# Performance work log

Measured on AMD Instinct MI355X. Metric: run time of the kernel, lower is better.

Reference implementation:

```python
import jax, jax.numpy as jnp
import numpy as np

TOPK_CONF = 100   # cfg.nms_top_k_conf
TOPK_IOU = 15     # cfg.nms_top_k_iou
IOU_GAUSS = (32, 32)  # cfg.iou_gauss_dim
EPS = 1e-6        # cfg.positive


def unnormal_gaussian(mask_shape, loc):
    """loc: [..., 4] = (cx, cy, w, h) in [0,1). Returns [..., H, W] unnormalized gaussians."""
    H, W = mask_shape
    ys = (jnp.arange(H, dtype=loc.dtype) + 0.5) / H  # [H]
    xs = (jnp.arange(W, dtype=loc.dtype) + 0.5) / W  # [W]
    cx, cy = loc[..., 0], loc[..., 1]
    sx = jnp.abs(loc[..., 2]) * 0.5 + 1e-3
    sy = jnp.abs(loc[..., 3]) * 0.5 + 1e-3
    dx2 = (xs - cx[..., None]) ** 2 / (2.0 * sx[..., None] ** 2)  # [..., W]
    dy2 = (ys - cy[..., None]) ** 2 / (2.0 * sy[..., None] ** 2)  # [..., H]
    return jnp.exp(-(dy2[..., :, None] + dx2[..., None, :]))      # [..., H, W]


def setup_inputs() -> dict:
    key = jax.random.key(0)
    k1, k2, k3, k4, k5 = jax.random.split(key, 5)
    B, P, C, M = 4, 19248, 81, 32
    original = jax.random.normal(k1, (B, 3, 550, 550), dtype=jnp.float32)
    loc = jax.random.uniform(k2, (B, P, 4), dtype=jnp.float32)  # cx,cy,w,h in [0,1)
    conf = jax.random.normal(k3, (B, P, C), dtype=jnp.float32)
    mask = jax.random.normal(k4, (B, P, M), dtype=jnp.float32)
    proto = jax.random.normal(k5, (B, 138, 138, M), dtype=jnp.float32)
    return {"original": original, "loc": loc, "conf": conf, "mask": mask, "proto": proto}


def reference(original, loc, conf, mask, proto):
    B, H, W = original.shape[0], original.shape[2], original.shape[3]
    # class-1 foreground confidence after softmax over classes
    conf1 = jax.nn.softmax(conf, axis=2)[:, :, 1]  # [B, P]

    # ---- detect(): top-k by conf, pairwise gaussian IoU, keep lowest-overlap boxes ----
    order = jnp.argsort(-conf1, axis=-1)[:, :TOPK_CONF]                    # [B, K]
    sconf = jnp.take_along_axis(conf1, order, axis=1)                      # [B, K]
    sloc = jnp.take_along_axis(loc, order[..., None], axis=1)              # [B, K, 4]
    smask = jnp.take_along_axis(mask, order[..., None], axis=1)            # [B, K, Mdim]

    gauss = unnormal_gaussian(IOU_GAUSS, sloc)                             # [B, K, G, G]
    g_rows = gauss[:, None, :, :, :]                                       # broadcast [B,1,K,G,G]
    g_cols = gauss[:, :, None, :, :]                                       # broadcast [B,K,1,G,G]
    inter = jnp.sum(jnp.minimum(g_rows, g_cols), axis=(-2, -1))            # [B, K, K]
    union = jnp.sum(jnp.maximum(g_rows, g_cols), axis=(-2, -1))            # [B, K, K]
    gauss_iou = inter / union
    iou_max = jnp.max(jnp.triu(gauss_iou, k=1), axis=1)                    # [B, K]
    keep = jnp.argsort(iou_max, axis=-1)[:, :TOPK_IOU]                     # [B, Kk]

    kloc = jnp.take_along_axis(sloc, keep[..., None], axis=1)              # [B, Kk, 4]
    kmask = jnp.take_along_axis(smask, keep[..., None], axis=1)            # [B, Kk, Mdim]
    kconf = jnp.take_along_axis(sconf, keep, axis=1)                       # [B, Kk]

    # ---- VarianceLoss ----
    Hp, Wp = proto.shape[1], proto.shape[2]
    ug = unnormal_gaussian((Hp, Wp), kloc)                                 # [B, Kk, Hp, Wp]
    assembled = jax.nn.sigmoid(jnp.einsum('bhwm,bkm->bkhw', proto, kmask)) # lincomb + sigmoid
    attention = assembled * ug
    mask_conf = attention * kconf[:, :, None, None]                        # einsum('abcd,ab->abcd')
    denom = jnp.sum(mask_conf, axis=1, keepdims=True) + EPS
    final_conf = 1.0 - jnp.sum(mask_conf ** 2 / denom, axis=1)             # [B, Hp, Wp]
    final_conf = jnp.where(jnp.isnan(final_conf), 0.0, final_conf)

    resized = jax.image.resize(final_conf, (B, H, W), method='bilinear')   # [B, H, W]
    total_conf = jnp.sum(resized, axis=0)                                  # [H, W]
    weighted_mean = jnp.einsum('bchw,bhw->chw', original, resized)         # [C, H, W]
    squared_diff = (original - weighted_mean) ** 2
    weighted_diff = squared_diff * resized[:, None, :, :]                  # einsum('abcd,acd->abcd')
    weighted_var = weighted_diff / (total_conf + EPS)
    return jnp.sum(weighted_var) / 100.0
```

## Files before the change

### kernel.cpp

```cpp
#include <hip/hip_runtime.h>
#include <math.h>

#define B 4
#define P 19248
#define C 81
#define M 32
#define K1 100
#define K2 15
#define G 32
#define HP 138
#define HO 550
#define FEPS 1e-6f
#define NLOC 19

#define NBUCKET 8192
#define CAP 2048

#define TI 16
#define NT 7
#define NTP 28
#define CH 128
#define NCH 8
#define SP 132

__global__ void k_conf1(const float* __restrict__ conf, float* __restrict__ conf1) {
    int gid  = blockIdx.x * blockDim.x + threadIdx.x;
    int wave = gid >> 6;
    int lane = threadIdx.x & 63;
    if (wave >= B * P) return;
    const float* row = conf + (size_t)wave * C;
    float x0 = (lane < C)      ? row[lane]      : -INFINITY;
    float x1 = (lane + 64 < C) ? row[lane + 64] : -INFINITY;
    float m = fmaxf(x0, x1);
#pragma unroll
    for (int o = 32; o; o >>= 1) m = fmaxf(m, __shfl_xor(m, o, 64));
    float s = 0.f;
    if (lane < C)      s += expf(x0 - m);
    if (lane + 64 < C) s += expf(x1 - m);
#pragma unroll
    for (int o = 32; o; o >>= 1) s += __shfl_xor(s, o, 64);
    if (lane == 0) conf1[wave] = expf(row[1] - m) / s;
}

__global__ __launch_bounds__(1024) void k_top100(
    const float* __restrict__ conf1, const float* __restrict__ loc,
    const float* __restrict__ mask,
    float* __restrict__ sconf, float* __restrict__ sloc,
    float* __restrict__ smask) {
    int b = blockIdx.x;
    int tid = threadIdx.x;
    const float* c1 = conf1 + (size_t)b * P;

    __shared__ unsigned int hist[NBUCKET];
    __shared__ unsigned int gsum_[1024];
    __shared__ unsigned int g2[64];
    __shared__ unsigned long long keys[CAP];
    __shared__ int s_T;
    __shared__ int s_cnt;
    __shared__ int   s_order[K1];
    __shared__ float s_conf[K1];

    for (int i = tid; i < NBUCKET; i += 1024) hist[i] = 0;
    if (tid == 0) s_cnt = 0;
    __syncthreads();

    unsigned int mybits[NLOC];
#pragma unroll
    for (int s = 0; s < NLOC; ++s) {
        int p = tid + s * 1024;
        mybits[s] = (p < P) ? __float_as_uint(c1[p]) : 0u;
        if (p < P) atomicAdd(&hist[mybits[s] >> 17], 1u);
    }
    __syncthreads();

    {
        unsigned int gs = 0;
#pragma unroll
        for (int i = 0; i < 8; ++i) gs += hist[tid * 8 + i];
        gsum_[tid] = gs;
    }
    __syncthreads();
    if (tid < 64) {
        unsigned int gs = 0;
#pragma unroll
        for (int i = 0; i < 16; ++i) gs += gsum_[tid * 16 + i];
        g2[tid] = gs;
    }
    __syncthreads();

    if (tid == 0) {
        int cum = 0;
        int S = 63;
        for (; S > 0; --S) {
            if (cum + (int)g2[S] >= K1) break;
            cum += (int)g2[S];
        }
        int gI = S * 16 + 15;
        for (; gI > S * 16; --gI) {
            if (cum + (int)gsum_[gI] >= K1) break;
            cum += (int)gsum_[gI];
        }
        int T = gI * 8 + 7;
        for (; T > gI * 8; --T) {
            cum += (int)hist[T];
            if (cum >= K1) break;
        }
        s_T = T;
    }
    __syncthreads();

    int T = s_T;
#pragma unroll
    for (int s = 0; s < NLOC; ++s) {
        int p = tid + s * 1024;
        if (p < P && (int)(mybits[s] >> 17) >= T) {
            int pos = atomicAdd(&s_cnt, 1);
            if (pos < CAP)
                keys[pos] = ((unsigned long long)mybits[s] << 32)
                          | (unsigned int)(0xFFFFFFFFu - (unsigned int)p);
        }
    }
    __syncthreads();
    int nc = min(s_cnt, CAP);

    if (tid < nc) {
        unsigned long long mk = keys[tid];
        int rank = 0;
        for (int i = 0; i < nc; ++i) rank += (keys[i] > mk);
        if (rank < K1) {
            unsigned int bits = (unsigned int)(mk >> 32);
            int idx = (int)(0xFFFFFFFFu - (unsigned int)(mk & 0xFFFFFFFFu));
            s_order[rank] = idx;
            s_conf[rank] = __uint_as_float(bits);
        }
    }
    __syncthreads();

    for (int t = tid; t < K1; t += 1024) {
        sconf[b * K1 + t] = s_conf[t];
    }
    for (int t = tid; t < K1 * 4; t += 1024) {
        int k = t >> 2, d = t & 3;
        sloc[(b * K1 + k) * 4 + d] = loc[((size_t)b * P + s_order[k]) * 4 + d];
    }
    for (int t = tid; t < K1 * M; t += 1024) {
        int k = t >> 5, d = t & 31;
        smask[(b * K1 + k) * M + d] = mask[((size_t)b * P + s_order[k]) * M + d];
    }
}

__global__ void k_gauss(const float* __restrict__ sloc, float* __restrict__ gauss,
                        unsigned int* __restrict__ ioumax, float* __restrict__ out) {
    int bk = blockIdx.x;
    if (threadIdx.x == 0) ioumax[bk] = 0u;
    if (bk == 0 && threadIdx.x == 1) out[0] = 0.f;
    const float* l = sloc + bk * 4;
    float cx = l[0], cy = l[1];
    float sx = fabsf(l[2]) * 0.5f + 0.001f;
    float sy = fabsf(l[3]) * 0.5f + 0.001f;
    float dsx = 2.f * sx * sx;
    float dsy = 2.f * sy * sy;
    for (int p = threadIdx.x; p < G * G; p += 256) {
        int y = p >> 5, x = p & 31;
        float xs = (x + 0.5f) / (float)G;
        float ys = (y + 0.5f) / (float)G;
        float dx2 = (xs - cx) * (xs - cx) / dsx;
        float dy2 = (ys - cy) * (ys - cy) / dsy;
        gauss[(size_t)bk * (G * G) + p] = expf(-(dy2 + dx2));
    }
}

__global__ __launch_bounds__(256) void k_iou(
    const float* __restrict__ gauss, unsigned int* __restrict__ ioumax) {
    int tp = blockIdx.x;
    int b  = blockIdx.y;
    int ti = 0, rem = tp;
    while (rem >= NT - ti) { rem -= NT - ti; ++ti; }
    int tj = ti + rem;

    __shared__ __align__(16) float As[TI][SP];
    __shared__ __align__(16) float Bs[TI][SP];

    int tid = threadIdx.x;
    int li = tid >> 4, lj = tid & 15;
    int i = ti * TI + li, j = tj * TI + lj;

    float inter = 0.f, uni = 0.f;
    for (int ch = 0; ch < NCH; ++ch) {
        __syncthreads();
        for (int idx = tid; idx < TI * (CH / 4); idx += 256) {
            int g = idx >> 5, v = idx & 31;
            int gi = ti * TI + g;
            float4 f = make_float4(0.f, 0.f, 0.f, 0.f);
            if (gi < K1)
                f = *(const float4*)(gauss + ((size_t)(b * K1 + gi) << 10) + ch * CH + v * 4);
            *(float4*)(&As[g][v * 4]) = f;
            int gj = tj * TI + g;
            float4 h = make_float4(0.f, 0.f, 0.f, 0.f);
            if (gj < K1)
                h = *(const float4*)(gauss + ((size_t)(b * K1 + gj) << 10) + ch * CH + v * 4);
            *(float4*)(&Bs[g][v * 4]) = h;
        }
        __syncthreads();
        const float4* ar = (const float4*)(&As[li][0]);
        const float4* br = (const float4*)(&Bs[lj][0]);
#pragma unroll
        for (int p = 0; p < CH / 4; ++p) {
            float4 a = ar[p], c = br[p];
            inter += fminf(a.x, c.x) + fminf(a.y, c.y)
                   + fminf(a.z, c.z) + fminf(a.w, c.w);
            uni   += fmaxf(a.x, c.x) + fmaxf(a.y, c.y)
                   + fmaxf(a.z, c.z) + fmaxf(a.w, c.w);
        }
    }
    if (i < j && j < K1) {
        float iou = inter / uni;
        atomicMax(&ioumax[b * K1 + j], __float_as_uint(iou));
    }
}

__global__ void k_keep(const unsigned int* __restrict__ ioumax,
                       const float* __restrict__ sloc, const float* __restrict__ smask,
                       const float* __restrict__ sconf,
                       float* __restrict__ kloc, float* __restrict__ kmask,
                       float* __restrict__ kconf) {
    int b = blockIdx.x;
    int lane = threadIdx.x;
    float v0 = (lane < K1)      ? __uint_as_float(ioumax[b * K1 + lane])      : INFINITY;
    float v1 = (lane + 64 < K1) ? __uint_as_float(ioumax[b * K1 + lane + 64]) : INFINITY;
    __shared__ int s_keep[K2];
    for (int k = 0; k < K2; ++k) {
        float bv; int bi;
        if (v0 <= v1) { bv = v0; bi = lane; }
        else          { bv = v1; bi = lane + 64; }
#pragma unroll
        for (int o = 32; o; o >>= 1) {
            float ov = __shfl_xor(bv, o, 64);
            int   oi = __shfl_xor(bi, o, 64);
            if (ov < bv || (ov == bv && oi < bi)) { bv = ov; bi = oi; }
        }
        if (bi == lane)           v0 = INFINITY;
        else if (bi == lane + 64) v1 = INFINITY;
        if (lane == 0) s_keep[k] = bi;
    }
    __syncthreads();
    for (int t = lane; t < K2 * M; t += 64) {
        int k = t >> 5, d = t & 31;
        kmask[(b * K2 + k) * M + d] = smask[(b * K1 + s_keep[k]) * M + d];
    }
    for (int t = lane; t < K2 * 4; t += 64) {
        int k = t >> 2, d = t & 3;
        kloc[(b * K2 + k) * 4 + d] = sloc[(b * K1 + s_keep[k]) * 4 + d];
    }
    if (lane < K2) kconf[b * K2 + lane] = sconf[b * K1 + s_keep[lane]];
}

__global__ __launch_bounds__(256) void k_fconf(
    const float* __restrict__ proto, const float* __restrict__ kloc,
    const float* __restrict__ kmask, const float* __restrict__ kconf,
    float* __restrict__ fconf) {
    int b = blockIdx.y;
    int px0 = blockIdx.x * 256;
    int tid = threadIdx.x;
    __shared__ float s_pv[256][M + 1];
    __shared__ float s_km[K2][M];
    __shared__ float s_loc[K2][4];
    __shared__ float s_cf[K2];
    for (int t = tid; t < K2 * M; t += 256) s_km[t >> 5][t & 31] = kmask[b * K2 * M + t];
    for (int t = tid; t < K2 * 4; t += 256) s_loc[t >> 2][t & 3] = kloc[b * K2 * 4 + t];
    if (tid < K2) s_cf[tid] = kconf[b * K2 + tid];

    int nvalid = min(256, HP * HP - px0);
    const float4* pr4 = (const float4*)(proto + ((size_t)b * (HP * HP) + px0) * M);
    for (int idx = tid; idx < nvalid * (M / 4); idx += 256) {
        float4 f = pr4[idx];
        int q = idx >> 3, v = idx & 7;
        s_pv[q][v * 4 + 0] = f.x;
        s_pv[q][v * 4 + 1] = f.y;
        s_pv[q][v * 4 + 2] = f.z;
        s_pv[q][v * 4 + 3] = f.w;
    }
    __syncthreads();

    if (tid < nvalid) {
        int p = px0 + tid;
        int h = p / HP, w = p % HP;
        float pv[M];
#pragma unroll
        for (int m = 0; m < M; ++m) pv[m] = s_pv[tid][m];
        float ys = (h + 0.5f) / (float)HP;
        float xs = (w + 0.5f) / (float)HP;
        float sum_a = 0.f, sum_a2 = 0.f;
#pragma unroll 1
        for (int k = 0; k < K2; ++k) {
            float d = 0.f;
#pragma unroll
            for (int m = 0; m < M; ++m) d += pv[m] * s_km[k][m];
            float sig = 1.f / (1.f + expf(-d));
            float cx = s_loc[k][0], cy = s_loc[k][1];
            float sx = fabsf(s_loc[k][2]) * 0.5f + 0.001f;
            float sy = fabsf(s_loc[k][3]) * 0.5f + 0.001f;
            float dx2 = (xs - cx) * (xs - cx) / (2.f * sx * sx);
            float dy2 = (ys - cy) * (ys - cy) / (2.f * sy * sy);
            float ug = expf(-(dy2 + dx2));
            float a = sig * ug * s_cf[k];
            sum_a  += a;
            sum_a2 += a * a;
        }
        float fin = 1.f - sum_a2 / (sum_a + FEPS);
        if (!(fin == fin)) fin = 0.f;
        fconf[(size_t)b * HP * HP + p] = fin;
    }
}

__global__ void k_reduce(const float* __restrict__ fconf, const float* __restrict__ original,
                         float* __restrict__ out) {
    int idx = blockIdx.x * 256 + threadIdx.x;
    float contrib = 0.f;
    if (idx < HO * HO) {
        int y = idx / HO, x = idx % HO;
        const float scale = (float)HP / (float)HO;
        float fy = (y + 0.5f) * scale - 0.5f;
        float fx = (x + 0.5f) * scale - 0.5f;
        float y0f = floorf(fy), x0f = floorf(fx);
        float wy = fy - y0f, wx = fx - x0f;
        int y0 = (int)y0f, x0 = (int)x0f;
        int iy0 = max(y0, 0), iy1 = min(y0 + 1, HP - 1);
        int ix0 = max(x0, 0), ix1 = min(x0 + 1, HP - 1);
        float r[B];
#pragma unroll
        for (int b = 0; b < B; ++b) {
            const float* F = fconf + (size_t)b * HP * HP;
            float v00 = F[iy0 * HP + ix0], v01 = F[iy0 * HP + ix1];
            float v10 = F[iy1 * HP + ix0], v11 = F[iy1 * HP + ix1];
            r[b] = (1.f - wy) * ((1.f - wx) * v00 + wx * v01)
                 +        wy  * ((1.f - wx) * v10 + wx * v11);
        }
        float t = r[0] + r[1] + r[2] + r[3];
        float s = 0.f;
#pragma unroll
        for (int c = 0; c < 3; ++c) {
            float o[B], wm = 0.f;
#pragma unroll
            for (int b = 0; b < B; ++b) {
                o[b] = original[(((size_t)b * 3 + c) * HO + y) * HO + x];
                wm += o[b] * r[b];
            }
#pragma unroll
            for (int b = 0; b < B; ++b) {
                float d = o[b] - wm;
                s += d * d * r[b];
            }
        }
        contrib = s / (t + FEPS);
    }
    __shared__ float red[256];
    red[threadIdx.x] = contrib;
    __syncthreads();
    for (int off = 128; off; off >>= 1) {
        if (threadIdx.x < off) red[threadIdx.x] += red[threadIdx.x + off];
        __syncthreads();
    }
    if (threadIdx.x == 0) atomicAdd(out, red[0] * 0.01f);
}

extern "C" void kernel_launch(void* const* d_in, const int* in_sizes, int n_in,
                              void* d_out, int out_size, void* d_ws, size_t ws_size,
                              hipStream_t stream) {
    (void)in_sizes; (void)n_in; (void)out_size; (void)ws_size;
    const float* original = (const float*)d_in[0];
    const float* loc      = (const float*)d_in[1];
    const float* conf     = (const float*)d_in[2];
    const float* mask     = (const float*)d_in[3];
    const float* proto    = (const float*)d_in[4];
    float* out = (float*)d_out;

    char* ws = (char*)d_ws;
    size_t off = 0;
    auto alloc = [&](size_t bytes) -> void* {
        void* p = ws + off;
        off += (bytes + 255) & ~(size_t)255;
        return p;
    };
    float* conf1        = (float*)alloc((size_t)B * P * sizeof(float));
    float* sconf        = (float*)alloc((size_t)B * K1 * sizeof(float));
    float* sloc         = (float*)alloc((size_t)B * K1 * 4 * sizeof(float));
    float* smask        = (float*)alloc((size_t)B * K1 * M * sizeof(float));
    float* gauss        = (float*)alloc((size_t)B * K1 * G * G * sizeof(float));
    unsigned int* iomax = (unsigned int*)alloc((size_t)B * K1 * sizeof(unsigned int));
    float* kloc         = (float*)alloc((size_t)B * K2 * 4 * sizeof(float));
    float* kmask        = (float*)alloc((size_t)B * K2 * M * sizeof(float));
    float* kconf        = (float*)alloc((size_t)B * K2 * sizeof(float));
    float* fconf        = (float*)alloc((size_t)B * HP * HP * sizeof(float));

    k_conf1<<<(B * P) / 4, 256, 0, stream>>>(conf, conf1);
    k_top100<<<B, 1024, 0, stream>>>(conf1, loc, mask, sconf, sloc, smask);
    k_gauss<<<B * K1, 256, 0, stream>>>(sloc, gauss, iomax, out);
    dim3 g4(NTP, B);
    k_iou<<<g4, 256, 0, stream>>>(gauss, iomax);
    k_keep<<<B, 64, 0, stream>>>(iomax, sloc, smask, sconf, kloc, kmask, kconf);
    dim3 g6((HP * HP + 255) / 256, B);
    k_fconf<<<g6, 256, 0, stream>>>(proto, kloc, kmask, kconf, fconf);
    k_reduce<<<(HO * HO + 255) / 256, 256, 0, stream>>>(fconf, original, out);
}
```

Measured before the change: 188.0 us.

## Fuse gaussian generation into IoU kernel and keep-selection into fconf kernel

Drops the standalone gaussian kernel: each IoU tile now computes its gaussian values on the fly in shared memory from the box parameters, so the gauss buffer no longer goes through global memory. The top-15 keep selection moves into the start of every fconf block, and ioumax/out zeroing moves into the conf1 kernel. This removes two kernel launches and the intermediate buffers. In exchange the exp work is repeated across tiles and every fconf block repeats the selection.

```diff
diff --git a/kernel.cpp b/kernel.cpp
--- a/kernel.cpp
+++ b/kernel.cpp
@@ -23,7 +23,12 @@
 #define NCH 8
 #define SP 132
 
-__global__ void k_conf1(const float* __restrict__ conf, float* __restrict__ conf1) {
+__global__ void k_conf1(const float* __restrict__ conf, float* __restrict__ conf1,
+                        unsigned int* __restrict__ ioumax, float* __restrict__ out) {
+    if (blockIdx.x == 0) {
+        for (int t = threadIdx.x; t < B * K1; t += 256) ioumax[t] = 0u;
+        if (threadIdx.x == 0) out[0] = 0.f;
+    }
     int gid  = blockIdx.x * blockDim.x + threadIdx.x;
     int wave = gid >> 6;
     int lane = threadIdx.x & 63;
@@ -149,29 +154,8 @@
     }
 }
 
-__global__ void k_gauss(const float* __restrict__ sloc, float* __restrict__ gauss,
-                        unsigned int* __restrict__ ioumax, float* __restrict__ out) {
-    int bk = blockIdx.x;
-    if (threadIdx.x == 0) ioumax[bk] = 0u;
-    if (bk == 0 && threadIdx.x == 1) out[0] = 0.f;
-    const float* l = sloc + bk * 4;
-    float cx = l[0], cy = l[1];
-    float sx = fabsf(l[2]) * 0.5f + 0.001f;
-    float sy = fabsf(l[3]) * 0.5f + 0.001f;
-    float dsx = 2.f * sx * sx;
-    float dsy = 2.f * sy * sy;
-    for (int p = threadIdx.x; p < G * G; p += 256) {
-        int y = p >> 5, x = p & 31;
-        float xs = (x + 0.5f) / (float)G;
-        float ys = (y + 0.5f) / (float)G;
-        float dx2 = (xs - cx) * (xs - cx) / dsx;
-        float dy2 = (ys - cy) * (ys - cy) / dsy;
-        gauss[(size_t)bk * (G * G) + p] = expf(-(dy2 + dx2));
-    }
-}
-
 __global__ __launch_bounds__(256) void k_iou(
-    const float* __restrict__ gauss, unsigned int* __restrict__ ioumax) {
+    const float* __restrict__ sloc, unsigned int* __restrict__ ioumax) {
     int tp = blockIdx.x;
     int b  = blockIdx.y;
     int ti = 0, rem = tp;
@@ -180,26 +164,51 @@
 
     __shared__ __align__(16) float As[TI][SP];
     __shared__ __align__(16) float Bs[TI][SP];
+    __shared__ float pa[2][TI][4];
 
     int tid = threadIdx.x;
+    if (tid < 2 * TI) {
+        int which = tid >> 4, g = tid & 15;
+        int gi = (which ? tj : ti) * TI + g;
+        float cx = 0.f, cy = 0.f, dsx = 1.f, dsy = 1.f;
+        if (gi < K1) {
+            const float* l = sloc + (size_t)(b * K1 + gi) * 4;
+            cx = l[0]; cy = l[1];
+            float sx = fabsf(l[2]) * 0.5f + 0.001f;
+            float sy = fabsf(l[3]) * 0.5f + 0.001f;
+            dsx = 2.f * sx * sx;
+            dsy = 2.f * sy * sy;
+        }
+        pa[which][g][0] = cx; pa[which][g][1] = cy;
+        pa[which][g][2] = dsx; pa[which][g][3] = dsy;
+    }
+
     int li = tid >> 4, lj = tid & 15;
     int i = ti * TI + li, j = tj * TI + lj;
 
     float inter = 0.f, uni = 0.f;
     for (int ch = 0; ch < NCH; ++ch) {
         __syncthreads();
-        for (int idx = tid; idx < TI * (CH / 4); idx += 256) {
-            int g = idx >> 5, v = idx & 31;
-            int gi = ti * TI + g;
-            float4 f = make_float4(0.f, 0.f, 0.f, 0.f);
-            if (gi < K1)
-                f = *(const float4*)(gauss + ((size_t)(b * K1 + gi) << 10) + ch * CH + v * 4);
-            *(float4*)(&As[g][v * 4]) = f;
-            int gj = tj * TI + g;
-            float4 h = make_float4(0.f, 0.f, 0.f, 0.f);
-            if (gj < K1)
-                h = *(const float4*)(gauss + ((size_t)(b * K1 + gj) << 10) + ch * CH + v * 4);
-            *(float4*)(&Bs[g][v * 4]) = h;
+#pragma unroll
+        for (int t = 0; t < TI * CH / 256; ++t) {
+            int idx = tid + t * 256;
+            int g = idx >> 7, px = idx & 127;
+            int p = ch * CH + px;
+            int y = p >> 5, x = p & 31;
+            float xs = (x + 0.5f) / (float)G;
+            float ys = (y + 0.5f) / (float)G;
+            {
+                float cx = pa[0][g][0], cy = pa[0][g][1];
+                float dx2 = (xs - cx) * (xs - cx) / pa[0][g][2];
+                float dy2 = (ys - cy) * (ys - cy) / pa[0][g][3];
+                As[g][px] = expf(-(dy2 + dx2));
+            }
+            {
+                float cx = pa[1][g][0], cy = pa[1][g][1];
+                float dx2 = (xs - cx) * (xs - cx) / pa[1][g][2];
+                float dy2 = (ys - cy) * (ys - cy) / pa[1][g][3];
+                Bs[g][px] = expf(-(dy2 + dx2));
+            }
         }
         __syncthreads();
         const float4* ar = (const float4*)(&As[li][0]);
@@ -219,46 +228,10 @@
     }
 }
 
-__global__ void k_keep(const unsigned int* __restrict__ ioumax,
-                       const float* __restrict__ sloc, const float* __restrict__ smask,
-                       const float* __restrict__ sconf,
-                       float* __restrict__ kloc, float* __restrict__ kmask,
-                       float* __restrict__ kconf) {
-    int b = blockIdx.x;
-    int lane = threadIdx.x;
-    float v0 = (lane < K1)      ? __uint_as_float(ioumax[b * K1 + lane])      : INFINITY;
-    float v1 = (lane + 64 < K1) ? __uint_as_float(ioumax[b * K1 + lane + 64]) : INFINITY;
-    __shared__ int s_keep[K2];
-    for (int k = 0; k < K2; ++k) {
-        float bv; int bi;
-        if (v0 <= v1) { bv = v0; bi = lane; }
-        else          { bv = v1; bi = lane + 64; }
-#pragma unroll
-        for (int o = 32; o; o >>= 1) {
-            float ov = __shfl_xor(bv, o, 64);
-            int   oi = __shfl_xor(bi, o, 64);
-            if (ov < bv || (ov == bv && oi < bi)) { bv = ov; bi = oi; }
-        }
-        if (bi == lane)           v0 = INFINITY;
-        else if (bi == lane + 64) v1 = INFINITY;
-        if (lane == 0) s_keep[k] = bi;
-    }
-    __syncthreads();
-    for (int t = lane; t < K2 * M; t += 64) {
-        int k = t >> 5, d = t & 31;
-        kmask[(b * K2 + k) * M + d] = smask[(b * K1 + s_keep[k]) * M + d];
-    }
-    for (int t = lane; t < K2 * 4; t += 64) {
-        int k = t >> 2, d = t & 3;
-        kloc[(b * K2 + k) * 4 + d] = sloc[(b * K1 + s_keep[k]) * 4 + d];
-    }
-    if (lane < K2) kconf[b * K2 + lane] = sconf[b * K1 + s_keep[lane]];
-}
-
 __global__ __launch_bounds__(256) void k_fconf(
-    const float* __restrict__ proto, const float* __restrict__ kloc,
-    const float* __restrict__ kmask, const float* __restrict__ kconf,
-    float* __restrict__ fconf) {
+    const float* __restrict__ proto, const unsigned int* __restrict__ ioumax,
+    const float* __restrict__ sloc, const float* __restrict__ smask,
+    const float* __restrict__ sconf, float* __restrict__ fconf) {
     int b = blockIdx.y;
     int px0 = blockIdx.x * 256;
     int tid = threadIdx.x;
@@ -266,9 +239,38 @@
     __shared__ float s_km[K2][M];
     __shared__ float s_loc[K2][4];
     __shared__ float s_cf[K2];
-    for (int t = tid; t < K2 * M; t += 256) s_km[t >> 5][t & 31] = kmask[b * K2 * M + t];
-    for (int t = tid; t < K2 * 4; t += 256) s_loc[t >> 2][t & 3] = kloc[b * K2 * 4 + t];
-    if (tid < K2) s_cf[tid] = kconf[b * K2 + tid];
+    __shared__ int s_keep[K2];
+
+    if (tid < 64) {
+        int lane = tid;
+        float v0 = (lane < K1)      ? __uint_as_float(ioumax[b * K1 + lane])      : INFINITY;
+        float v1 = (lane + 64 < K1) ? __uint_as_float(ioumax[b * K1 + lane + 64]) : INFINITY;
+        for (int k = 0; k < K2; ++k) {
+            float bv; int bi;
+            if (v0 <= v1) { bv = v0; bi = lane; }
+            else          { bv = v1; bi = lane + 64; }
+#pragma unroll
+            for (int o = 32; o; o >>= 1) {
+                float ov = __shfl_xor(bv, o, 64);
+                int   oi = __shfl_xor(bi, o, 64);
+                if (ov < bv || (ov == bv && oi < bi)) { bv = ov; bi = oi; }
+            }
+            if (bi == lane)           v0 = INFINITY;
+            else if (bi == lane + 64) v1 = INFINITY;
+            if (lane == 0) s_keep[k] = bi;
+        }
+    }
+    __syncthreads();
+
+    for (int t = tid; t < K2 * M; t += 256) {
+        int k = t >> 5, d = t & 31;
+        s_km[k][d] = smask[(b * K1 + s_keep[k]) * M + d];
+    }
+    for (int t = tid; t < K2 * 4; t += 256) {
+        int k = t >> 2, d = t & 3;
+        s_loc[k][d] = sloc[(b * K1 + s_keep[k]) * 4 + d];
+    }
+    if (tid < K2) s_cf[tid] = sconf[b * K1 + s_keep[tid]];
 
     int nvalid = min(256, HP * HP - px0);
     const float4* pr4 = (const float4*)(proto + ((size_t)b * (HP * HP) + px0) * M);
@@ -386,20 +388,14 @@
     float* sconf        = (float*)alloc((size_t)B * K1 * sizeof(float));
     float* sloc         = (float*)alloc((size_t)B * K1 * 4 * sizeof(float));
     float* smask        = (float*)alloc((size_t)B * K1 * M * sizeof(float));
-    float* gauss        = (float*)alloc((size_t)B * K1 * G * G * sizeof(float));
     unsigned int* iomax = (unsigned int*)alloc((size_t)B * K1 * sizeof(unsigned int));
-    float* kloc         = (float*)alloc((size_t)B * K2 * 4 * sizeof(float));
-    float* kmask        = (float*)alloc((size_t)B * K2 * M * sizeof(float));
-    float* kconf        = (float*)alloc((size_t)B * K2 * sizeof(float));
     float* fconf        = (float*)alloc((size_t)B * HP * HP * sizeof(float));
 
-    k_conf1<<<(B * P) / 4, 256, 0, stream>>>(conf, conf1);
+    k_conf1<<<(B * P) / 4, 256, 0, stream>>>(conf, conf1, iomax, out);
     k_top100<<<B, 1024, 0, stream>>>(conf1, loc, mask, sconf, sloc, smask);
-    k_gauss<<<B * K1, 256, 0, stream>>>(sloc, gauss, iomax, out);
     dim3 g4(NTP, B);
-    k_iou<<<g4, 256, 0, stream>>>(gauss, iomax);
-    k_keep<<<B, 64, 0, stream>>>(iomax, sloc, smask, sconf, kloc, kmask, kconf);
+    k_iou<<<g4, 256, 0, stream>>>(sloc, iomax);
     dim3 g6((HP * HP + 255) / 256, B);
-    k_fconf<<<g6, 256, 0, stream>>>(proto, kloc, kmask, kconf, fconf);
+    k_fconf<<<g6, 256, 0, stream>>>(proto, iomax, sloc, smask, sconf, fconf);
     k_reduce<<<(HO * HO + 255) / 256, 256, 0, stream>>>(fconf, original, out);
 }
```

Result: no change. 191.4 us (+1.8%).

## Split IoU tiles across chunks, fuse keep-selection into fconf, move init

Applied to the files above, without the earlier changes.

The pairwise IoU kernel now launches one block per (chunk, tile, batch), which raises the block count eightfold. Each block writes partial intersection/union sums to a buffer, and a new combine kernel reduces them and applies atomicMax. The separate k_keep kernel is removed: every k_fconf block recomputes the top-15 lowest-IoU selection and gathers masks, locations and confidences directly. Zeroing of ioumax and out moves into k_conf1. The net kernel count stays the same, and the cost is an extra partial buffer plus redundant selection work in every fconf block.

```diff
diff --git a/kernel.cpp b/kernel.cpp
--- a/kernel.cpp
+++ b/kernel.cpp
@@ -23,7 +23,12 @@
 #define NCH 8
 #define SP 132
 
-__global__ void k_conf1(const float* __restrict__ conf, float* __restrict__ conf1) {
+__global__ void k_conf1(const float* __restrict__ conf, float* __restrict__ conf1,
+                        unsigned int* __restrict__ ioumax, float* __restrict__ out) {
+    if (blockIdx.x == 0) {
+        for (int t = threadIdx.x; t < B * K1; t += 256) ioumax[t] = 0u;
+        if (threadIdx.x == 0) out[0] = 0.f;
+    }
     int gid  = blockIdx.x * blockDim.x + threadIdx.x;
     int wave = gid >> 6;
     int lane = threadIdx.x & 63;
@@ -149,11 +154,8 @@
     }
 }
 
-__global__ void k_gauss(const float* __restrict__ sloc, float* __restrict__ gauss,
-                        unsigned int* __restrict__ ioumax, float* __restrict__ out) {
+__global__ void k_gauss(const float* __restrict__ sloc, float* __restrict__ gauss) {
     int bk = blockIdx.x;
-    if (threadIdx.x == 0) ioumax[bk] = 0u;
-    if (bk == 0 && threadIdx.x == 1) out[0] = 0.f;
     const float* l = sloc + bk * 4;
     float cx = l[0], cy = l[1];
     float sx = fabsf(l[2]) * 0.5f + 0.001f;
@@ -170,10 +172,11 @@
     }
 }
 
-__global__ __launch_bounds__(256) void k_iou(
-    const float* __restrict__ gauss, unsigned int* __restrict__ ioumax) {
-    int tp = blockIdx.x;
-    int b  = blockIdx.y;
+__global__ __launch_bounds__(256) void k_iou_tile(
+    const float* __restrict__ gauss, float2* __restrict__ pbuf) {
+    int ch = blockIdx.x;
+    int tp = blockIdx.y;
+    int b  = blockIdx.z;
     int ti = 0, rem = tp;
     while (rem >= NT - ti) { rem -= NT - ti; ++ti; }
     int tj = ti + rem;
@@ -182,83 +185,65 @@
     __shared__ __align__(16) float Bs[TI][SP];
 
     int tid = threadIdx.x;
+    for (int idx = tid; idx < TI * (CH / 4); idx += 256) {
+        int g = idx >> 5, v = idx & 31;
+        int gi = ti * TI + g;
+        float4 f = make_float4(0.f, 0.f, 0.f, 0.f);
+        if (gi < K1)
+            f = *(const float4*)(gauss + ((size_t)(b * K1 + gi) << 10) + ch * CH + v * 4);
+        *(float4*)(&As[g][v * 4]) = f;
+        int gj = tj * TI + g;
+        float4 h = make_float4(0.f, 0.f, 0.f, 0.f);
+        if (gj < K1)
+            h = *(const float4*)(gauss + ((size_t)(b * K1 + gj) << 10) + ch * CH + v * 4);
+        *(float4*)(&Bs[g][v * 4]) = h;
+    }
+    __syncthreads();
+
+    int li = tid >> 4, lj = tid & 15;
+    const float4* ar = (const float4*)(&As[li][0]);
+    const float4* br = (const float4*)(&Bs[lj][0]);
+    float inter = 0.f, uni = 0.f;
+#pragma unroll
+    for (int p = 0; p < CH / 4; ++p) {
+        float4 a = ar[p], c = br[p];
+        inter += fminf(a.x, c.x) + fminf(a.y, c.y)
+               + fminf(a.z, c.z) + fminf(a.w, c.w);
+        uni   += fmaxf(a.x, c.x) + fmaxf(a.y, c.y)
+               + fmaxf(a.z, c.z) + fmaxf(a.w, c.w);
+    }
+    pbuf[(((size_t)(b * NTP + tp)) * NCH + ch) * 256 + tid] = make_float2(inter, uni);
+}
+
+__global__ __launch_bounds__(256) void k_combine(
+    const float2* __restrict__ pbuf, unsigned int* __restrict__ ioumax) {
+    int tp = blockIdx.x;
+    int b  = blockIdx.y;
+    int tid = threadIdx.x;
+    int ti = 0, rem = tp;
+    while (rem >= NT - ti) { rem -= NT - ti; ++ti; }
+    int tj = ti + rem;
     int li = tid >> 4, lj = tid & 15;
     int i = ti * TI + li, j = tj * TI + lj;
 
-    float inter = 0.f, uni = 0.f;
+    size_t base = ((size_t)(b * NTP + tp)) * NCH * 256 + tid;
+    float I = 0.f, U = 0.f;
+#pragma unroll
     for (int ch = 0; ch < NCH; ++ch) {
-        __syncthreads();
-        for (int idx = tid; idx < TI * (CH / 4); idx += 256) {
-            int g = idx >> 5, v = idx & 31;
-            int gi = ti * TI + g;
-            float4 f = make_float4(0.f, 0.f, 0.f, 0.f);
-            if (gi < K1)
-                f = *(const float4*)(gauss + ((size_t)(b * K1 + gi) << 10) + ch * CH + v * 4);
-            *(float4*)(&As[g][v * 4]) = f;
-            int gj = tj * TI + g;
-            float4 h = make_float4(0.f, 0.f, 0.f, 0.f);
-            if (gj < K1)
-                h = *(const float4*)(gauss + ((size_t)(b * K1 + gj) << 10) + ch * CH + v * 4);
-            *(float4*)(&Bs[g][v * 4]) = h;
-        }
-        __syncthreads();
-        const float4* ar = (const float4*)(&As[li][0]);
-        const float4* br = (const float4*)(&Bs[lj][0]);
-#pragma unroll
-        for (int p = 0; p < CH / 4; ++p) {
-            float4 a = ar[p], c = br[p];
-            inter += fminf(a.x, c.x) + fminf(a.y, c.y)
-                   + fminf(a.z, c.z) + fminf(a.w, c.w);
-            uni   += fmaxf(a.x, c.x) + fmaxf(a.y, c.y)
-                   + fmaxf(a.z, c.z) + fmaxf(a.w, c.w);
-        }
+        float2 f = pbuf[base + (size_t)ch * 256];
+        I += f.x;
+        U += f.y;
     }
     if (i < j && j < K1) {
-        float iou = inter / uni;
+        float iou = I / U;
         atomicMax(&ioumax[b * K1 + j], __float_as_uint(iou));
     }
 }
 
-__global__ void k_keep(const unsigned int* __restrict__ ioumax,
-                       const float* __restrict__ sloc, const float* __restrict__ smask,
-                       const float* __restrict__ sconf,
-                       float* __restrict__ kloc, float* __restrict__ kmask,
-                       float* __restrict__ kconf) {
-    int b = blockIdx.x;
-    int lane = threadIdx.x;
-    float v0 = (lane < K1)      ? __uint_as_float(ioumax[b * K1 + lane])      : INFINITY;
-    float v1 = (lane + 64 < K1) ? __uint_as_float(ioumax[b * K1 + lane + 64]) : INFINITY;
-    __shared__ int s_keep[K2];
-    for (int k = 0; k < K2; ++k) {
-        float bv; int bi;
-        if (v0 <= v1) { bv = v0; bi = lane; }
-        else          { bv = v1; bi = lane + 64; }
-#pragma unroll
-        for (int o = 32; o; o >>= 1) {
-            float ov = __shfl_xor(bv, o, 64);
-            int   oi = __shfl_xor(bi, o, 64);
-            if (ov < bv || (ov == bv && oi < bi)) { bv = ov; bi = oi; }
-        }
-        if (bi == lane)           v0 = INFINITY;
-        else if (bi == lane + 64) v1 = INFINITY;
-        if (lane == 0) s_keep[k] = bi;
-    }
-    __syncthreads();
-    for (int t = lane; t < K2 * M; t += 64) {
-        int k = t >> 5, d = t & 31;
-        kmask[(b * K2 + k) * M + d] = smask[(b * K1 + s_keep[k]) * M + d];
-    }
-    for (int t = lane; t < K2 * 4; t += 64) {
-        int k = t >> 2, d = t & 3;
-        kloc[(b * K2 + k) * 4 + d] = sloc[(b * K1 + s_keep[k]) * 4 + d];
-    }
-    if (lane < K2) kconf[b * K2 + lane] = sconf[b * K1 + s_keep[lane]];
-}
-
 __global__ __launch_bounds__(256) void k_fconf(
-    const float* __restrict__ proto, const float* __restrict__ kloc,
-    const float* __restrict__ kmask, const float* __restrict__ kconf,
-    float* __restrict__ fconf) {
+    const float* __restrict__ proto, const unsigned int* __restrict__ ioumax,
+    const float* __restrict__ sloc, const float* __restrict__ smask,
+    const float* __restrict__ sconf, float* __restrict__ fconf) {
     int b = blockIdx.y;
     int px0 = blockIdx.x * 256;
     int tid = threadIdx.x;
@@ -266,9 +251,38 @@
     __shared__ float s_km[K2][M];
     __shared__ float s_loc[K2][4];
     __shared__ float s_cf[K2];
-    for (int t = tid; t < K2 * M; t += 256) s_km[t >> 5][t & 31] = kmask[b * K2 * M + t];
-    for (int t = tid; t < K2 * 4; t += 256) s_loc[t >> 2][t & 3] = kloc[b * K2 * 4 + t];
-    if (tid < K2) s_cf[tid] = kconf[b * K2 + tid];
+    __shared__ int s_keep[K2];
+
+    if (tid < 64) {
+        int lane = tid;
+        float v0 = (lane < K1)      ? __uint_as_float(ioumax[b * K1 + lane])      : INFINITY;
+        float v1 = (lane + 64 < K1) ? __uint_as_float(ioumax[b * K1 + lane + 64]) : INFINITY;
+        for (int k = 0; k < K2; ++k) {
+            float bv; int bi;
+            if (v0 <= v1) { bv = v0; bi = lane; }
+            else          { bv = v1; bi = lane + 64; }
+#pragma unroll
+            for (int o = 32; o; o >>= 1) {
+                float ov = __shfl_xor(bv, o, 64);
+                int   oi = __shfl_xor(bi, o, 64);
+                if (ov < bv || (ov == bv && oi < bi)) { bv = ov; bi = oi; }
+            }
+            if (bi == lane)           v0 = INFINITY;
+            else if (bi == lane + 64) v1 = INFINITY;
+            if (lane == 0) s_keep[k] = bi;
+        }
+    }
+    __syncthreads();
+
+    for (int t = tid; t < K2 * M; t += 256) {
+        int k = t >> 5, d = t & 31;
+        s_km[k][d] = smask[(b * K1 + s_keep[k]) * M + d];
+    }
+    for (int t = tid; t < K2 * 4; t += 256) {
+        int k = t >> 2, d = t & 3;
+        s_loc[k][d] = sloc[(b * K1 + s_keep[k]) * 4 + d];
+    }
+    if (tid < K2) s_cf[tid] = sconf[b * K1 + s_keep[tid]];
 
     int nvalid = min(256, HP * HP - px0);
     const float4* pr4 = (const float4*)(proto + ((size_t)b * (HP * HP) + px0) * M);
@@ -387,19 +401,18 @@
     float* sloc         = (float*)alloc((size_t)B * K1 * 4 * sizeof(float));
     float* smask        = (float*)alloc((size_t)B * K1 * M * sizeof(float));
     float* gauss        = (float*)alloc((size_t)B * K1 * G * G * sizeof(float));
+    float2* pbuf        = (float2*)alloc((size_t)B * NTP * NCH * 256 * sizeof(float2));
     unsigned int* iomax = (unsigned int*)alloc((size_t)B * K1 * sizeof(unsigned int));
-    float* kloc         = (float*)alloc((size_t)B * K2 * 4 * sizeof(float));
-    float* kmask        = (float*)alloc((size_t)B * K2 * M * sizeof(float));
-    float* kconf        = (float*)alloc((size_t)B * K2 * sizeof(float));
     float* fconf        = (float*)alloc((size_t)B * HP * HP * sizeof(float));
 
-    k_conf1<<<(B * P) / 4, 256, 0, stream>>>(conf, conf1);
+    k_conf1<<<(B * P) / 4, 256, 0, stream>>>(conf, conf1, iomax, out);
     k_top100<<<B, 1024, 0, stream>>>(conf1, loc, mask, sconf, sloc, smask);
-    k_gauss<<<B * K1, 256, 0, stream>>>(sloc, gauss, iomax, out);
-    dim3 g4(NTP, B);
-    k_iou<<<g4, 256, 0, stream>>>(gauss, iomax);
-    k_keep<<<B, 64, 0, stream>>>(iomax, sloc, smask, sconf, kloc, kmask, kconf);
+    k_gauss<<<B * K1, 256, 0, stream>>>(sloc, gauss);
+    dim3 g4(NCH, NTP, B);
+    k_iou_tile<<<g4, 256, 0, stream>>>(gauss, pbuf);
+    dim3 g4b(NTP, B);
+    k_combine<<<g4b, 256, 0, stream>>>(pbuf, iomax);
     dim3 g6((HP * HP + 255) / 256, B);
-    k_fconf<<<g6, 256, 0, stream>>>(proto, kloc, kmask, kconf, fconf);
+    k_fconf<<<g6, 256, 0, stream>>>(proto, iomax, sloc, smask, sconf, fconf);
     k_reduce<<<(HO * HO + 255) / 256, 256, 0, stream>>>(fconf, original, out);
 }
```

Result: faster. 167.3 us (-11.0%).
